# Performance work log

Hardware: AMD Instinct MI355X
Metric: run time of the kernel (lower is better)

## Reference

```python
import jax, jax.numpy as jnp
import numpy as np

C = 256      # channels
G = 8        # groups
K = 9        # 3x3 sampling points (DCNv4 default kernel_size=3)
DWK = 3      # dw_kernel_size (wrapper passes kernel_size=3)
OFFSET_SCALE = 1.0
N, H, W = 8, 64, 64


def setup_inputs() -> dict:
    key = jax.random.key(0)
    ks = jax.random.split(key, 6)
    def init(k, shape, fan):
        return jax.random.normal(k, shape, jnp.float32) * (fan ** -0.5)
    return {
        "x": jax.random.normal(ks[0], (N, C, H, W), jnp.float32),
        "dw_w": init(ks[1], (C, 1, DWK, DWK), DWK * DWK),   # depthwise conv (OIHW, groups=C)
        "dw_b": jnp.zeros((C,), jnp.float32),
        "om_w": init(ks[2], (G * K * 3, C), C) * 0.01,       # offset/mask linear (small offsets)
        "om_b": jnp.zeros((G * K * 3,), jnp.float32),
        "vp_w": init(ks[3], (C, C), C),                      # value_proj
        "vp_b": jnp.zeros((C,), jnp.float32),
        "op_w": init(ks[4], (C, C), C),                      # output_proj (output_bias=False)
    }


def reference(x, dw_w, dw_b, om_w, om_b, vp_w, vp_b, op_w):
    n, c, h, w = x.shape
    cg = c // G
    L = h * w
    # b c h w -> b (h w) c
    xf = x.transpose(0, 2, 3, 1).reshape(n, L, c)
    value = (xf @ vp_w.T + vp_b).reshape(n, L, G, cg)
    # offset/mask branch: depthwise conv on raw input, then linear
    om_in = jax.lax.conv_general_dilated(
        x, dw_w, (1, 1), "SAME", feature_group_count=c,
        dimension_numbers=("NCHW", "OIHW", "NCHW")) + dw_b[None, :, None, None]
    om = om_in.transpose(0, 2, 3, 1).reshape(n, L, c) @ om_w.T + om_b  # (n, L, G*K*3)
    om = om.reshape(n, h, w, G, K * 3)
    off = om[..., : 2 * K].reshape(n, h, w, G, K, 2) * OFFSET_SCALE     # (dy, dx) per point
    mask = om[..., 2 * K:]                                              # (n,h,w,G,K) raw (DCNv4: no softmax)
    # base 3x3 dilation-1 grid centered at each pixel
    d = jnp.arange(-1, 2, dtype=jnp.float32)
    dy, dx = jnp.meshgrid(d, d, indexing="ij")
    base = jnp.stack([dy.ravel(), dx.ravel()], -1)  # (K, 2)
    py = (jnp.arange(h, dtype=jnp.float32).reshape(1, h, 1, 1, 1)
          + base[:, 0].reshape(1, 1, 1, 1, K) + off[..., 0])  # (n,h,w,G,K)
    px = (jnp.arange(w, dtype=jnp.float32).reshape(1, 1, w, 1, 1)
          + base[:, 1].reshape(1, 1, 1, 1, K) + off[..., 1])
    y0 = jnp.floor(py); x0 = jnp.floor(px)
    ty = py - y0; tx = px - x0
    y0i = y0.astype(jnp.int32); x0i = x0.astype(jnp.int32)

    def gather(yi, xi, wgt):
        valid = (yi >= 0) & (yi < h) & (xi >= 0) & (xi < w)
        idx = jnp.clip(yi, 0, h - 1) * w + jnp.clip(xi, 0, w - 1)       # (n,h,w,G,K)
        idx = idx.transpose(0, 1, 2, 4, 3).reshape(n, L * K, G)[..., None]
        g = jnp.take_along_axis(value, idx, axis=1)                     # (n, L*K, G, cg)
        g = g.reshape(n, h, w, K, G, cg).transpose(0, 1, 2, 4, 3, 5)    # (n,h,w,G,K,cg)
        return g * (wgt * valid)[..., None]

    sampled = (gather(y0i,     x0i,     (1 - ty) * (1 - tx))
             + gather(y0i,     x0i + 1, (1 - ty) * tx)
             + gather(y0i + 1, x0i,     ty * (1 - tx))
             + gather(y0i + 1, x0i + 1, ty * tx))
    out = jnp.einsum("nhwgk,nhwgkc->nhwgc", mask, sampled)  # mask-weighted aggregation
    out = out.reshape(n, L, c) @ op_w.T                      # output_proj (no bias)
    # b (h w) c -> b c h w
    return out.reshape(n, h, w, c).transpose(0, 3, 1, 2)
```

## Files before the change

### kernel.cpp

```cpp
#include <hip/hip_runtime.h>
#include <math.h>

#define N_  8
#define C_  256
#define G_  8
#define CG_ 32
#define K_  9
#define H_  64
#define W_  64
#define L_  (H_*W_)
#define OM_ 216
#define OMP_ 256

using frag_ab = __attribute__((ext_vector_type(8))) short;
using frag_cd = __attribute__((ext_vector_type(4))) float;

__device__ __forceinline__ unsigned short f2bf(float f) {
    unsigned int u = __float_as_uint(f);
    u += 0x7FFFu + ((u >> 16) & 1u);
    return (unsigned short)(u >> 16);
}
__device__ __forceinline__ float bflo(unsigned int u) { return __uint_as_float(u << 16); }
__device__ __forceinline__ float bfhi(unsigned int u) { return __uint_as_float(u & 0xFFFF0000u); }

__device__ __forceinline__ void gld16(const void* g, void* l) {
    __builtin_amdgcn_global_load_lds((const __attribute__((address_space(1))) void*)g,
                                     (__attribute__((address_space(3))) void*)l, 16, 0, 0);
}

__global__ __launch_bounds__(256) void prep_kernel(const float* __restrict__ x,
                                                   const float* __restrict__ w,
                                                   const float* __restrict__ b,
                                                   const float* __restrict__ vp_w,
                                                   const float* __restrict__ om_w,
                                                   const float* __restrict__ om_b,
                                                   const float* __restrict__ op_w,
                                                   unsigned short* __restrict__ xb,
                                                   unsigned short* __restrict__ omb,
                                                   unsigned short* __restrict__ vp_wb,
                                                   unsigned short* __restrict__ om_wb,
                                                   float* __restrict__ om_bp,
                                                   unsigned short* __restrict__ op_wb) {
    const int n = blockIdx.z, y0 = blockIdx.y * 4, c0 = blockIdx.x * 32;
    const int tid = threadIdx.x;
    __shared__ float xs[6][32][66];
    __shared__ __align__(16) unsigned short os[2][64][40];
    for (int i = tid; i < 384; i += 256) {
        int r = i / 64, c = (i / 2) % 32, e = i & 1;
        xs[r][c][e * 65] = 0.f;
    }
    const float* xbase = x + ((size_t)n * C_ + c0) * L_;
    for (int i = tid; i < 6 * 32 * 16; i += 256) {
        int r = i >> 9, rem = i & 511, c = rem >> 4, x4 = (rem & 15) * 4;
        int yy = y0 + r - 1;
        float4 v = make_float4(0.f, 0.f, 0.f, 0.f);
        if ((unsigned)yy < (unsigned)H_) v = *(const float4*)(xbase + (size_t)c * L_ + yy * W_ + x4);
        xs[r][c][1 + x4] = v.x; xs[r][c][2 + x4] = v.y;
        xs[r][c][3 + x4] = v.z; xs[r][c][4 + x4] = v.w;
    }
    __syncthreads();

    const int c = tid & 31, x0 = (tid >> 5) * 8;
    float wv[9];
#pragma unroll
    for (int i = 0; i < 9; i++) wv[i] = w[(c0 + c) * 9 + i];
    const float bias = b[c0 + c];
    const int l = tid >> 2, c8 = (tid & 3) * 8;

    for (int rr = 0; rr < 4; rr++) {
        float o[8];
#pragma unroll
        for (int j = 0; j < 8; j++) o[j] = bias;
#pragma unroll
        for (int r = 0; r < 3; r++) {
            float v[10];
#pragma unroll
            for (int d = 0; d < 10; d++) v[d] = xs[rr + r][c][x0 + d];
#pragma unroll
            for (int j = 0; j < 8; j++)
                o[j] += wv[r * 3] * v[j] + wv[r * 3 + 1] * v[j + 1] + wv[r * 3 + 2] * v[j + 2];
        }
#pragma unroll
        for (int j = 0; j < 8; j++) {
            os[0][x0 + j][c] = f2bf(xs[rr + 1][c][1 + x0 + j]);
            os[1][x0 + j][c] = f2bf(o[j]);
        }
        __syncthreads();
        uint4 va = *(const uint4*)&os[0][l][c8];
        uint4 vc = *(const uint4*)&os[1][l][c8];
        size_t dst = (((size_t)n * 8 + blockIdx.x) * L_ + (y0 + rr) * W_ + l) * 32 + c8;
        *(uint4*)(xb + dst) = va;
        *(uint4*)(omb + dst) = vc;
        __syncthreads();
    }

    if (n == 0) {
        int base = (blockIdx.x + 8 * blockIdx.y) * 256 + tid;
#pragma unroll
        for (int rep2 = 0; rep2 < 2; rep2++) {
            int idx = base + rep2 * 32768;
            vp_wb[idx] = f2bf(vp_w[idx]);
            op_wb[idx] = f2bf(op_w[idx]);
            om_wb[idx] = (idx < OM_ * C_) ? f2bf(om_w[idx]) : (unsigned short)0;
        }
        if (base < OMP_) om_bp[base] = (base < OM_) ? om_b[base] : 0.f;
    }
}

__global__ __launch_bounds__(256) void gemm12_kernel(const unsigned short* __restrict__ xb,
                                                     const unsigned short* __restrict__ omb,
                                                     const unsigned short* __restrict__ vp_wb,
                                                     const unsigned short* __restrict__ om_wb,
                                                     const float* __restrict__ vp_b,
                                                     const float* __restrict__ om_bp,
                                                     unsigned short* __restrict__ valueb,
                                                     float* __restrict__ omf) {
    __shared__ unsigned short As[128 * 32];
    __shared__ unsigned short Bs[128 * 32];
    const int which = blockIdx.z;
    const unsigned short* A = which ? omb : xb;
    const unsigned short* B = which ? om_wb : vp_wb;
    const float* bias = which ? om_bp : vp_b;
    const int tid = threadIdx.x;
    const long i0 = (long)blockIdx.x * 128;
    const long j0 = (long)blockIdx.y * 128;
    const int nA = (int)(i0 >> 12);
    const int lofs = (int)(i0 & 4095);
    const unsigned short* Bb = B + j0 * C_;
    const int wave = tid >> 6, lane = tid & 63;
    const int iw = (wave & 1) * 64, jw = (wave >> 1) * 64;
    const int lm = lane & 15, kq = lane >> 4;
    const int srow = tid >> 2, scol = (tid & 3) * 8;

    frag_cd acc[4][4];
#pragma unroll
    for (int a = 0; a < 4; a++)
#pragma unroll
        for (int c = 0; c < 4; c++) acc[a][c] = (frag_cd){0.f, 0.f, 0.f, 0.f};

    for (int k0 = 0; k0 < C_; k0 += 32) {
        const unsigned short* ga0 = A + (((size_t)nA * 8 + (k0 >> 5)) * L_ + lofs + srow) * 32 + scol;
        const unsigned short* gb0 = Bb + (long)srow * C_ + k0 + scol;
        gld16(ga0,            As + tid * 8);
        gld16(ga0 + 64 * 32,  As + 2048 + tid * 8);
        gld16(gb0,            Bs + tid * 8);
        gld16(gb0 + 64 * C_,  Bs + 2048 + tid * 8);
        __syncthreads();
        frag_ab af[4], bfr[4];
#pragma unroll
        for (int mi = 0; mi < 4; mi++)
            af[mi] = *(const frag_ab*)&As[(iw + mi * 16 + lm) * 32 + kq * 8];
#pragma unroll
        for (int ni = 0; ni < 4; ni++)
            bfr[ni] = *(const frag_ab*)&Bs[(jw + ni * 16 + lm) * 32 + kq * 8];
#pragma unroll
        for (int mi = 0; mi < 4; mi++)
#pragma unroll
            for (int ni = 0; ni < 4; ni++)
                acc[mi][ni] = __builtin_amdgcn_mfma_f32_16x16x32_bf16(af[mi], bfr[ni], acc[mi][ni], 0, 0, 0);
        __syncthreads();
    }

    float bv[4];
#pragma unroll
    for (int ni = 0; ni < 4; ni++)
        bv[ni] = bias[(int)(j0 + jw + ni * 16 + lm)];

    const long ibase = i0 + iw + kq * 4;
    const long jbase = j0 + jw + lm;
#pragma unroll
    for (int mi = 0; mi < 4; mi++) {
#pragma unroll
        for (int ni = 0; ni < 4; ni++) {
            long j = jbase + ni * 16;
#pragma unroll
            for (int r = 0; r < 4; r++) {
                long i = ibase + mi * 16 + r;
                float v = acc[mi][ni][r] + bv[ni];
                if (which)
                    omf[i * OMP_ + j] = v;
                else
                    valueb[i * C_ + j] = f2bf(v);
            }
        }
    }
}

__global__ __launch_bounds__(256, 2) void samplegemm_kernel(const unsigned short* __restrict__ value,
                                                            const float* __restrict__ om,
                                                            const unsigned short* __restrict__ opw,
                                                            float* __restrict__ out) {
    const int n = blockIdx.x, l0 = blockIdx.y * 64;
    const int tid = threadIdx.x;
    __shared__ __align__(16) unsigned short interm[64 * 256];
    __shared__ float4 wgt[64][9];
    __shared__ uint4  soff[64][9];

    const char* vbase = (const char*)(value + (size_t)n * L_ * C_);
    const int lp = tid >> 2;
    const int g = lp & 7;
    const int c8i = tid & 3;
    const int slot = tid & 31;
    const char* vb = vbase + (size_t)(g * CG_ + c8i * 8) * 2;

    for (int rep = 0; rep < 8; rep++) {
        __syncthreads();
        for (int it = tid; it < 576; it += 256) {
            int pl = it / 9, k = it - pl * 9;
            int p = rep * 8 + (pl >> 3), gg = pl & 7;
            int l = l0 + p, y = l >> 6, xp2 = l & 63;
            const float* so = om + ((size_t)n * L_ + l) * OMP_ + gg * 27;
            float offy = so[2 * k], offx = so[2 * k + 1], mk = so[18 + k];
            float py = (float)(y + k / 3 - 1) + offy;
            float px = (float)(xp2 + k % 3 - 1) + offx;
            float fy = floorf(py), fx = floorf(px);
            float ty = py - fy, tx = px - fx;
            int y0 = (int)fy, x0i = (int)fx;
            int y1 = y0 + 1, x1 = x0i + 1;
            float vy0 = ((unsigned)y0 < (unsigned)H_) ? 1.f : 0.f;
            float vy1 = ((unsigned)y1 < (unsigned)H_) ? 1.f : 0.f;
            float vx0 = ((unsigned)x0i < (unsigned)W_) ? 1.f : 0.f;
            float vx1 = ((unsigned)x1 < (unsigned)W_) ? 1.f : 0.f;
            int cy0 = min(max(y0, 0), H_ - 1), cy1 = min(max(y1, 0), H_ - 1);
            int cx0 = min(max(x0i, 0), W_ - 1), cx1 = min(max(x1, 0), W_ - 1);
            wgt[pl][k] = make_float4(mk * (1.f - ty) * (1.f - tx) * vy0 * vx0,
                                     mk * (1.f - ty) * tx         * vy0 * vx1,
                                     mk * ty         * (1.f - tx) * vy1 * vx0,
                                     mk * ty         * tx         * vy1 * vx1);
            soff[pl][k] = make_uint4((unsigned)((cy0 * W_ + cx0) << 9),
                                     (unsigned)((cy0 * W_ + cx1) << 9),
                                     (unsigned)((cy1 * W_ + cx0) << 9),
                                     (unsigned)((cy1 * W_ + cx1) << 9));
        }
        __syncthreads();
        const int p = rep * 8 + (lp >> 3);
        float acc[8] = {0.f, 0.f, 0.f, 0.f, 0.f, 0.f, 0.f, 0.f};
#pragma unroll
        for (int k = 0; k < K_; k++) {
            float4 wk = wgt[lp][k];
            uint4  ok = soff[lp][k];
            const uint4 v00 = *(const uint4*)(vb + ok.x);
            const uint4 v01 = *(const uint4*)(vb + ok.y);
            const uint4 v10 = *(const uint4*)(vb + ok.z);
            const uint4 v11 = *(const uint4*)(vb + ok.w);
#define ACC8(V, WW) { \
            acc[0] += WW * bflo(V.x); acc[1] += WW * bfhi(V.x); \
            acc[2] += WW * bflo(V.y); acc[3] += WW * bfhi(V.y); \
            acc[4] += WW * bflo(V.z); acc[5] += WW * bfhi(V.z); \
            acc[6] += WW * bflo(V.w); acc[7] += WW * bfhi(V.w); }
            ACC8(v00, wk.x) ACC8(v01, wk.y) ACC8(v10, wk.z) ACC8(v11, wk.w)
#undef ACC8
        }
        uint4 pk;
        unsigned short* ps = (unsigned short*)&pk;
#pragma unroll
        for (int i = 0; i < 8; i++) ps[i] = f2bf(acc[i]);
        int phys = slot ^ (p & 7);
        *(uint4*)&interm[p * 256 + phys * 8] = pk;
    }
    __syncthreads();

    const int wave = tid >> 6, lane = tid & 63;
    const int lm = lane & 15, kq = lane >> 4;
    const int q0w = wave * 64;
    frag_cd acc2[4][4];
#pragma unroll
    for (int a = 0; a < 4; a++)
#pragma unroll
        for (int c = 0; c < 4; c++) acc2[a][c] = (frag_cd){0.f, 0.f, 0.f, 0.f};

    for (int k0 = 0; k0 < C_; k0 += 32) {
        frag_ab af[4], bfr[4];
#pragma unroll
        for (int mi = 0; mi < 4; mi++)
            af[mi] = *(const frag_ab*)(opw + (size_t)(q0w + mi * 16 + lm) * C_ + k0 + kq * 8);
#pragma unroll
        for (int ni = 0; ni < 4; ni++) {
            int pxr = ni * 16 + lm;
            int phys = (k0 / 8 + kq) ^ (pxr & 7);
            bfr[ni] = *(const frag_ab*)&interm[pxr * 256 + phys * 8];
        }
#pragma unroll
        for (int mi = 0; mi < 4; mi++)
#pragma unroll
            for (int ni = 0; ni < 4; ni++)
                acc2[mi][ni] = __builtin_amdgcn_mfma_f32_16x16x32_bf16(af[mi], bfr[ni], acc2[mi][ni], 0, 0, 0);
    }

    float* ob = out + (size_t)n * C_ * L_ + l0;
#pragma unroll
    for (int mi = 0; mi < 4; mi++) {
#pragma unroll
        for (int ni = 0; ni < 4; ni++) {
            int pxr = ni * 16 + lm;
#pragma unroll
            for (int r = 0; r < 4; r++) {
                int q = q0w + mi * 16 + kq * 4 + r;
                ob[(size_t)q * L_ + pxr] = acc2[mi][ni][r];
            }
        }
    }
}

extern "C" void kernel_launch(void* const* d_in, const int* in_sizes, int n_in,
                              void* d_out, int out_size, void* d_ws, size_t ws_size,
                              hipStream_t stream) {
    const float* x    = (const float*)d_in[0];
    const float* dw_w = (const float*)d_in[1];
    const float* dw_b = (const float*)d_in[2];
    const float* om_w = (const float*)d_in[3];
    const float* om_b = (const float*)d_in[4];
    const float* vp_w = (const float*)d_in[5];
    const float* vp_b = (const float*)d_in[6];
    const float* op_w = (const float*)d_in[7];
    float* out = (float*)d_out;

    char* ws = (char*)d_ws;
    unsigned short* xb      = (unsigned short*)(ws);
    unsigned short* omb     = (unsigned short*)(ws + 16777216);
    unsigned short* valueb  = (unsigned short*)(ws + 33554432);
    float*          omf     = (float*)(ws + 50331648);
    unsigned short* vp_wb   = (unsigned short*)(ws + 83886080);
    unsigned short* om_wb   = (unsigned short*)(ws + 84017152);
    unsigned short* op_wb   = (unsigned short*)(ws + 84148224);
    float*          om_bp   = (float*)(ws + 84279296);

    prep_kernel<<<dim3(C_ / 32, H_ / 4, N_), 256, 0, stream>>>(
        x, dw_w, dw_b, vp_w, om_w, om_b, op_w,
        xb, omb, vp_wb, om_wb, om_bp, op_wb);
    gemm12_kernel<<<dim3(256, 2, 2), 256, 0, stream>>>(
        xb, omb, vp_wb, om_wb, vp_b, om_bp, valueb, omf);
    samplegemm_kernel<<<dim3(N_, L_ / 64), 256, 0, stream>>>(valueb, omf, op_wb, out);
}
```

Measured before the change: 174.1 us.

## Prefetch offset/mask rows per wave into LDS and drop block barriers

In the sampling+GEMM kernel, offset/mask rows for the next group of 8 pixels are now prefetched asynchronously into a per-wave LDS buffer with global_load_lds. Each wave computes the bilinear tap weights and offsets only for the pixels it consumes itself. This removes the two block-wide __syncthreads per iteration and hides the om load latency behind the bilinear gather. The trade-off is that correctness now depends on wave-local ownership and on manual vmcnt waits instead of full barriers.

```diff
diff --git a/kernel.cpp b/kernel.cpp
--- a/kernel.cpp
+++ b/kernel.cpp
@@ -26,6 +26,31 @@
 __device__ __forceinline__ void gld16(const void* g, void* l) {
     __builtin_amdgcn_global_load_lds((const __attribute__((address_space(1))) void*)g,
                                      (__attribute__((address_space(3))) void*)l, 16, 0, 0);
+}
+
+__device__ __forceinline__ void tapcalc(int l, int k, float offy, float offx, float mk,
+                                        float4& wq, uint4& sq) {
+    const int y = l >> 6, xp = l & 63;
+    float py = (float)(y + k / 3 - 1) + offy;
+    float px = (float)(xp + k % 3 - 1) + offx;
+    float fy = floorf(py), fx = floorf(px);
+    float ty = py - fy, tx = px - fx;
+    int y0 = (int)fy, x0i = (int)fx;
+    int y1 = y0 + 1, x1 = x0i + 1;
+    float vy0 = ((unsigned)y0 < (unsigned)H_) ? 1.f : 0.f;
+    float vy1 = ((unsigned)y1 < (unsigned)H_) ? 1.f : 0.f;
+    float vx0 = ((unsigned)x0i < (unsigned)W_) ? 1.f : 0.f;
+    float vx1 = ((unsigned)x1 < (unsigned)W_) ? 1.f : 0.f;
+    int cy0 = min(max(y0, 0), H_ - 1), cy1 = min(max(y1, 0), H_ - 1);
+    int cx0 = min(max(x0i, 0), W_ - 1), cx1 = min(max(x1, 0), W_ - 1);
+    wq = make_float4(mk * (1.f - ty) * (1.f - tx) * vy0 * vx0,
+                     mk * (1.f - ty) * tx         * vy0 * vx1,
+                     mk * ty         * (1.f - tx) * vy1 * vx0,
+                     mk * ty         * tx         * vy1 * vx1);
+    sq = make_uint4((unsigned)((cy0 * W_ + cx0) << 9),
+                    (unsigned)((cy0 * W_ + cx1) << 9),
+                    (unsigned)((cy1 * W_ + cx0) << 9),
+                    (unsigned)((cy1 * W_ + cx1) << 9));
 }
 
 __global__ __launch_bounds__(256) void prep_kernel(const float* __restrict__ x,
@@ -193,46 +218,50 @@
     const int n = blockIdx.x, l0 = blockIdx.y * 64;
     const int tid = threadIdx.x;
     __shared__ __align__(16) unsigned short interm[64 * 256];
+    __shared__ __align__(16) float ombuf[8][224];
     __shared__ float4 wgt[64][9];
     __shared__ uint4  soff[64][9];
 
-    const char* vbase = (const char*)(value + (size_t)n * L_ * C_);
+    const int wave = tid >> 6, lane = tid & 63;
     const int lp = tid >> 2;
     const int g = lp & 7;
     const int c8i = tid & 3;
     const int slot = tid & 31;
+    const char* vbase = (const char*)(value + (size_t)n * L_ * C_);
     const char* vb = vbase + (size_t)(g * CG_ + c8i * 8) * 2;
 
+    const float* omn = om + (size_t)n * L_ * OMP_;
+    float* obase = &ombuf[2 * wave][0];
+
+    const int s0row = (lane < 56) ? 0 : 1;
+    const int s0idx = (lane < 56) ? lane : (lane - 56);
+
+#define STAGE_OM(REP) { \
+        const float* r0_ = omn + (size_t)(l0 + (REP) * 8 + 2 * wave) * OMP_; \
+        gld16(r0_ + (size_t)s0row * OMP_ + s0idx * 4, obase); \
+        if (lane < 48) gld16(r0_ + OMP_ + (8 + lane) * 4, (char*)obase + 1024); }
+
+    STAGE_OM(0)
+
     for (int rep = 0; rep < 8; rep++) {
-        __syncthreads();
-        for (int it = tid; it < 576; it += 256) {
-            int pl = it / 9, k = it - pl * 9;
-            int p = rep * 8 + (pl >> 3), gg = pl & 7;
-            int l = l0 + p, y = l >> 6, xp2 = l & 63;
-            const float* so = om + ((size_t)n * L_ + l) * OMP_ + gg * 27;
-            float offy = so[2 * k], offx = so[2 * k + 1], mk = so[18 + k];
-            float py = (float)(y + k / 3 - 1) + offy;
-            float px = (float)(xp2 + k % 3 - 1) + offx;
-            float fy = floorf(py), fx = floorf(px);
-            float ty = py - fy, tx = px - fx;
-            int y0 = (int)fy, x0i = (int)fx;
-            int y1 = y0 + 1, x1 = x0i + 1;
-            float vy0 = ((unsigned)y0 < (unsigned)H_) ? 1.f : 0.f;
-            float vy1 = ((unsigned)y1 < (unsigned)H_) ? 1.f : 0.f;
-            float vx0 = ((unsigned)x0i < (unsigned)W_) ? 1.f : 0.f;
-            float vx1 = ((unsigned)x1 < (unsigned)W_) ? 1.f : 0.f;
-            int cy0 = min(max(y0, 0), H_ - 1), cy1 = min(max(y1, 0), H_ - 1);
-            int cx0 = min(max(x0i, 0), W_ - 1), cx1 = min(max(x1, 0), W_ - 1);
-            wgt[pl][k] = make_float4(mk * (1.f - ty) * (1.f - tx) * vy0 * vx0,
-                                     mk * (1.f - ty) * tx         * vy0 * vx1,
-                                     mk * ty         * (1.f - tx) * vy1 * vx0,
-                                     mk * ty         * tx         * vy1 * vx1);
-            soff[pl][k] = make_uint4((unsigned)((cy0 * W_ + cx0) << 9),
-                                     (unsigned)((cy0 * W_ + cx1) << 9),
-                                     (unsigned)((cy1 * W_ + cx0) << 9),
-                                     (unsigned)((cy1 * W_ + cx1) << 9));
-        }
-        __syncthreads();
+        asm volatile("s_waitcnt vmcnt(0)" ::: "memory");
+#pragma unroll
+        for (int j = 0; j < 3; j++) {
+            if (!(j == 2 && lane >= 16)) {
+                int it = lane + j * 64;
+                int pl_loc = it / 9, k = it - pl_loc * 9;
+                int pl = wave * 16 + pl_loc;
+                int pic = pl >> 3;
+                const float* ob2 = &ombuf[pic][(pl & 7) * 27];
+                float offy = ob2[2 * k], offx = ob2[2 * k + 1], mk = ob2[18 + k];
+                float4 wq; uint4 sq;
+                tapcalc(l0 + rep * 8 + pic, k, offy, offx, mk, wq, sq);
+                wgt[pl][k] = wq; soff[pl][k] = sq;
+            }
+        }
+        asm volatile("" ::: "memory");
+        if (rep < 7) STAGE_OM(rep + 1)
+        asm volatile("" ::: "memory");
         const int p = rep * 8 + (lp >> 3);
         float acc[8] = {0.f, 0.f, 0.f, 0.f, 0.f, 0.f, 0.f, 0.f};
 #pragma unroll
@@ -258,9 +287,9 @@
         int phys = slot ^ (p & 7);
         *(uint4*)&interm[p * 256 + phys * 8] = pk;
     }
+#undef STAGE_OM
     __syncthreads();
 
-    const int wave = tid >> 6, lane = tid & 63;
     const int lm = lane & 15, kq = lane >> 4;
     const int q0w = wave * 64;
     frag_cd acc2[4][4];
```

Result: faster. 170.5 us (-2.1%).
